# Performance work log

Hardware: AMD Instinct MI355X
Metric: run time of the kernel (lower is better)

## Reference

```python
import jax, jax.numpy as jnp
import numpy as np

# Faithful emulation of SQBnBLinear: SmoothQuant rescale fused with
# bnb Linear8bitLt (threshold=0.0 => no fp16 outlier path):
#   w_sq = weight / scales ; x_sq = x * scales
#   row-wise absmax int8 quantization of both x (per token) and w (per out row)
#   int8 GEMM, then dequant with (ax * aw / 127^2), plus bias / scales.

B, S, D = 4, 2048, 4096

def setup_inputs() -> dict:
    key = jax.random.key(0)
    k1, k2, k3, k4 = jax.random.split(key, 4)
    x = jax.random.normal(k1, (B, S, D), dtype=jnp.float32)
    weight = jax.random.normal(k2, (D, D), dtype=jnp.float32) * 0.02
    bias = jax.random.normal(k3, (D,), dtype=jnp.float32) * 0.02
    # SmoothQuant scales are positive per-input-channel factors
    scales = jax.random.uniform(k4, (D,), dtype=jnp.float32, minval=0.5, maxval=2.0)
    return {"x": x, "weight": weight, "bias": bias, "scales": scales}

def _quantize_rowwise(t):
    # symmetric per-row (last-dim) absmax int8 quantization
    absmax = jnp.max(jnp.abs(t), axis=-1, keepdims=True)
    absmax = jnp.maximum(absmax, 1e-8)
    q = jnp.clip(jnp.round(t * (127.0 / absmax)), -127.0, 127.0)
    return q, absmax

def reference(x, weight, bias, scales):
    # __init__: fold SmoothQuant scales into weight and bias
    w_sq = weight / scales            # [out, in] / [in]
    b_sq = bias / scales              # valid because in_features == out_features
    # forward: rescale input (mul_ by scales)
    x_sq = x * scales                 # [B, S, in]
    # LLM.int8() with threshold=0.0: pure int8 path
    qx, ax = _quantize_rowwise(x_sq)  # qx [B,S,in], ax [B,S,1]
    qw, aw = _quantize_rowwise(w_sq)  # qw [out,in], aw [out,1]
    acc = jnp.einsum('bsi,oi->bso', qx, qw)  # int accumulate (emulated in fp32)
    out = acc * (ax / 127.0) * (aw[:, 0] / 127.0) + b_sq
    return out
```

## Files before the change

kernel.cpp:

```cpp
#include <hip/hip_runtime.h>
#include <stdint.h>

#define DDIM 4096
#define MTOK 8192
#define KTILES (DDIM / 128)

typedef __attribute__((ext_vector_type(4))) int i32x4;
typedef __attribute__((ext_vector_type(16))) int i32x16;

__device__ __forceinline__ void async16(const void* g, void* l) {
    __builtin_amdgcn_global_load_lds(
        (const __attribute__((address_space(1))) unsigned int*)g,
        (__attribute__((address_space(3))) unsigned int*)l,
        16, 0, 0);
}

__global__ __launch_bounds__(256) void quant_all(
    const float* __restrict__ x, const float* __restrict__ weight,
    const float* __restrict__ scales,
    signed char* __restrict__ qx, float* __restrict__ sx,
    signed char* __restrict__ qw, float* __restrict__ sw,
    const float* __restrict__ bias, float* __restrict__ bq)
{
    __shared__ float red[4];
    const int tid = threadIdx.x;
    const bool is_x = blockIdx.x < MTOK;
    const int row = is_x ? blockIdx.x : (blockIdx.x - MTOK);
    const float* src = is_x ? (x + (size_t)row * DDIM) : (weight + (size_t)row * DDIM);
    signed char* q = is_x ? qx : qw;
    float* srow = is_x ? sx : sw;

    const float4* s4 = (const float4*)scales;
    const float4* x4 = (const float4*)src;

    float4 v[4];
    float am = 0.0f;
#pragma unroll
    for (int j = 0; j < 4; ++j) {
        float4 a = x4[tid + j * 256];
        float4 s = s4[tid + j * 256];
        float4 r;
        if (is_x) { r.x = a.x * s.x; r.y = a.y * s.y; r.z = a.z * s.z; r.w = a.w * s.w; }
        else      { r.x = a.x / s.x; r.y = a.y / s.y; r.z = a.z / s.z; r.w = a.w / s.w; }
        v[j] = r;
        am = fmaxf(am, fmaxf(fmaxf(fabsf(r.x), fabsf(r.y)),
                             fmaxf(fabsf(r.z), fabsf(r.w))));
    }
#pragma unroll
    for (int off = 32; off > 0; off >>= 1)
        am = fmaxf(am, __shfl_xor(am, off, 64));
    if ((tid & 63) == 0) red[tid >> 6] = am;
    __syncthreads();
    am = fmaxf(fmaxf(red[0], red[1]), fmaxf(red[2], red[3]));
    am = fmaxf(am, 1e-8f);

    const float sc = 127.0f / am;
    uint32_t* qrow = (uint32_t*)(q + (size_t)row * DDIM);
#pragma unroll
    for (int j = 0; j < 4; ++j) {
        int q0 = (int)fminf(127.0f, fmaxf(-127.0f, rintf(v[j].x * sc)));
        int q1 = (int)fminf(127.0f, fmaxf(-127.0f, rintf(v[j].y * sc)));
        int q2 = (int)fminf(127.0f, fmaxf(-127.0f, rintf(v[j].z * sc)));
        int q3 = (int)fminf(127.0f, fmaxf(-127.0f, rintf(v[j].w * sc)));
        qrow[tid + j * 256] = (uint32_t)(q0 & 0xff) | ((uint32_t)(q1 & 0xff) << 8) |
                              ((uint32_t)(q2 & 0xff) << 16) | ((uint32_t)(q3 & 0xff) << 24);
    }
    if (tid == 0) {
        srow[row] = am * (1.0f / 127.0f);
        if (!is_x) bq[row] = bias[row] / scales[row];
    }
}

__global__ __launch_bounds__(512, 2) void gemm_i8(
    const signed char* __restrict__ qx, const signed char* __restrict__ qw,
    const float* __restrict__ sx, const float* __restrict__ sw,
    const float* __restrict__ bq, float* __restrict__ out)
{
    __shared__ __align__(16) signed char sA[2][256 * 128];
    __shared__ __align__(16) signed char sB[2][256 * 128];

    const int K = DDIM, N = DDIM;
    const int tid  = threadIdx.x;
    const int bm   = blockIdx.y;
    const int bn   = blockIdx.x;
    const int wave = tid >> 6;
    const int lane = tid & 63;
    const int wm   = (wave >> 2) << 7;
    const int wn   = (wave & 3) << 6;
    const int r5   = lane & 31;
    const int hi   = lane >> 5;

    const signed char* Ab = qx + (size_t)bm * 256 * K;
    const signed char* Bb = qw + (size_t)bn * 256 * K;

    const int srow = tid >> 3;
    const int cir  = tid & 7;

    int roff[4];
#pragma unroll
    for (int kq = 0; kq < 4; ++kq)
        roff[kq] = (((kq * 2 + hi) ^ (r5 & 7)) << 4);

    i32x16 acc[4][2] = {};

#pragma unroll
    for (int c = 0; c < 4; ++c) {
        const int row = srow + 64 * c;
        const int kc  = cir ^ (row & 7);
        const int p   = tid * 16 + c * 8192;
        async16(Ab + (size_t)row * K + kc * 16, &sA[0][p]);
        async16(Bb + (size_t)row * K + kc * 16, &sB[0][p]);
    }

    for (int kt = 0; kt < KTILES; ++kt) {
        const int cur = kt & 1;

        if (kt + 1 < KTILES) {
            const int k0n = (kt + 1) * 128;
#pragma unroll
            for (int c = 0; c < 4; ++c) {
                const int row = srow + 64 * c;
                const int kc  = cir ^ (row & 7);
                const int p   = tid * 16 + c * 8192;
                async16(Ab + (size_t)row * K + k0n + kc * 16, &sA[cur ^ 1][p]);
                async16(Bb + (size_t)row * K + k0n + kc * 16, &sB[cur ^ 1][p]);
            }
            asm volatile("s_waitcnt vmcnt(8)" ::: "memory");
        } else {
            asm volatile("s_waitcnt vmcnt(0)" ::: "memory");
        }
        __builtin_amdgcn_s_barrier();
        __builtin_amdgcn_sched_barrier(0);

        const signed char* sAc = sA[cur];
        const signed char* sBc = sB[cur];

#pragma unroll
        for (int p = 0; p < 4; ++p) {
            i32x4 a0 = *(const i32x4*)&sAc[(wm +      r5) * 128 + roff[p]];
            i32x4 a1 = *(const i32x4*)&sAc[(wm + 32 + r5) * 128 + roff[p]];
            i32x4 a2 = *(const i32x4*)&sAc[(wm + 64 + r5) * 128 + roff[p]];
            i32x4 a3 = *(const i32x4*)&sAc[(wm + 96 + r5) * 128 + roff[p]];
            i32x4 b0 = *(const i32x4*)&sBc[(wn +      r5) * 128 + roff[p]];
            i32x4 b1 = *(const i32x4*)&sBc[(wn + 32 + r5) * 128 + roff[p]];

            __builtin_amdgcn_s_barrier();

            __builtin_amdgcn_s_setprio(1);
            acc[0][0] = __builtin_amdgcn_mfma_i32_32x32x32_i8(a0, b0, acc[0][0], 0, 0, 0);
            acc[0][1] = __builtin_amdgcn_mfma_i32_32x32x32_i8(a0, b1, acc[0][1], 0, 0, 0);
            acc[1][0] = __builtin_amdgcn_mfma_i32_32x32x32_i8(a1, b0, acc[1][0], 0, 0, 0);
            acc[1][1] = __builtin_amdgcn_mfma_i32_32x32x32_i8(a1, b1, acc[1][1], 0, 0, 0);
            acc[2][0] = __builtin_amdgcn_mfma_i32_32x32x32_i8(a2, b0, acc[2][0], 0, 0, 0);
            acc[2][1] = __builtin_amdgcn_mfma_i32_32x32x32_i8(a2, b1, acc[2][1], 0, 0, 0);
            acc[3][0] = __builtin_amdgcn_mfma_i32_32x32x32_i8(a3, b0, acc[3][0], 0, 0, 0);
            acc[3][1] = __builtin_amdgcn_mfma_i32_32x32x32_i8(a3, b1, acc[3][1], 0, 0, 0);
            __builtin_amdgcn_s_setprio(0);

            if (p < 3) __builtin_amdgcn_s_barrier();
        }
    }

#pragma unroll
    for (int mi = 0; mi < 4; ++mi) {
        const int mbase = bm * 256 + wm + mi * 32 + 4 * hi;
        float sxv[16];
#pragma unroll
        for (int r = 0; r < 16; ++r)
            sxv[r] = sx[mbase + (r & 3) + 8 * (r >> 2)];
#pragma unroll
        for (int nj = 0; nj < 2; ++nj) {
            const int n = bn * 256 + wn + nj * 32 + r5;
            const float swn = sw[n];
            const float bqn = bq[n];
#pragma unroll
            for (int r = 0; r < 16; ++r) {
                const int m = mbase + (r & 3) + 8 * (r >> 2);
                out[(size_t)m * N + n] = (float)acc[mi][nj][r] * sxv[r] * swn + bqn;
            }
        }
    }
}

extern "C" void kernel_launch(void* const* d_in, const int* in_sizes, int n_in,
                              void* d_out, int out_size, void* d_ws, size_t ws_size,
                              hipStream_t stream) {
    const float* x      = (const float*)d_in[0];
    const float* weight = (const float*)d_in[1];
    const float* bias   = (const float*)d_in[2];
    const float* scales = (const float*)d_in[3];
    float* out = (float*)d_out;

    char* ws = (char*)d_ws;
    signed char* qx = (signed char*)ws;
    signed char* qw = (signed char*)(ws + 33554432);
    float* sx = (float*)(ws + 50331648);
    float* sw = (float*)(ws + 50364416);
    float* bq = (float*)(ws + 50380800);

    quant_all<<<MTOK + DDIM, 256, 0, stream>>>(x, weight, scales, qx, sx, qw, sw, bias, bq);

    dim3 grid(DDIM / 256, MTOK / 256);
    gemm_i8<<<grid, 512, 0, stream>>>(qx, qw, sx, sw, bq, out);
}
```

Before: 422.9 us.

## Switch int8 GEMM to a 4-stage K=64 async ring with one barrier per tile

Replaces the double-buffered K=128 shared-memory pipeline with a four-slot ring of K=64 tiles that prefetches three tiles ahead. The XOR swizzle is adapted to 64-byte rows. Each tile now needs one barrier instead of several. All LDS fragment reads are issued up front, and the first MFMA group starts after a partial lgkmcnt wait, so LDS latency overlaps with matrix math. Total LDS use stays the same, but there are twice as many loop iterations, each with smaller tiles, and the manual vmcnt/lgkmcnt accounting must stay exact.

Measured after the change: 404.2 us. -4.4%, faster.

```diff
diff --git a/kernel.cpp b/kernel.cpp
--- a/kernel.cpp
+++ b/kernel.cpp
@@ -3,7 +3,7 @@
 
 #define DDIM 4096
 #define MTOK 8192
-#define KTILES (DDIM / 128)
+#define NT64 (DDIM / 64)
 
 typedef __attribute__((ext_vector_type(4))) int i32x4;
 typedef __attribute__((ext_vector_type(16))) int i32x16;
@@ -76,8 +76,8 @@
     const float* __restrict__ sx, const float* __restrict__ sw,
     const float* __restrict__ bq, float* __restrict__ out)
 {
-    __shared__ __align__(16) signed char sA[2][256 * 128];
-    __shared__ __align__(16) signed char sB[2][256 * 128];
+    __shared__ __align__(16) signed char sA[4][256 * 64];
+    __shared__ __align__(16) signed char sB[4][256 * 64];
 
     const int K = DDIM, N = DDIM;
     const int tid  = threadIdx.x;
@@ -89,77 +89,95 @@
     const int wn   = (wave & 3) << 6;
     const int r5   = lane & 31;
     const int hi   = lane >> 5;
+    const int xr   = (r5 >> 1) & 3;
 
     const signed char* Ab = qx + (size_t)bm * 256 * K;
     const signed char* Bb = qw + (size_t)bn * 256 * K;
 
-    const int srow = tid >> 3;
-    const int cir  = tid & 7;
-
-    int roff[4];
-#pragma unroll
-    for (int kq = 0; kq < 4; ++kq)
-        roff[kq] = (((kq * 2 + hi) ^ (r5 & 7)) << 4);
+    const int g_row = tid >> 2;
+    const int kc    = (tid & 3) ^ ((tid >> 3) & 3);
+    const int dst0  = tid * 16;
+
+    const int off0 = (((0 * 2 + hi) ^ xr) << 4);
+    const int off1 = (((1 * 2 + hi) ^ xr) << 4);
+    const int rA0 = (wm +      r5) * 64;
+    const int rA1 = (wm + 32 + r5) * 64;
+    const int rA2 = (wm + 64 + r5) * 64;
+    const int rA3 = (wm + 96 + r5) * 64;
+    const int rB0 = (wn +      r5) * 64;
+    const int rB1 = (wn + 32 + r5) * 64;
 
     i32x16 acc[4][2] = {};
 
-#pragma unroll
-    for (int c = 0; c < 4; ++c) {
-        const int row = srow + 64 * c;
-        const int kc  = cir ^ (row & 7);
-        const int p   = tid * 16 + c * 8192;
-        async16(Ab + (size_t)row * K + kc * 16, &sA[0][p]);
-        async16(Bb + (size_t)row * K + kc * 16, &sB[0][p]);
-    }
-
-    for (int kt = 0; kt < KTILES; ++kt) {
-        const int cur = kt & 1;
-
-        if (kt + 1 < KTILES) {
-            const int k0n = (kt + 1) * 128;
-#pragma unroll
-            for (int c = 0; c < 4; ++c) {
-                const int row = srow + 64 * c;
-                const int kc  = cir ^ (row & 7);
-                const int p   = tid * 16 + c * 8192;
-                async16(Ab + (size_t)row * K + k0n + kc * 16, &sA[cur ^ 1][p]);
-                async16(Bb + (size_t)row * K + k0n + kc * 16, &sB[cur ^ 1][p]);
-            }
-            asm volatile("s_waitcnt vmcnt(8)" ::: "memory");
-        } else {
-            asm volatile("s_waitcnt vmcnt(0)" ::: "memory");
-        }
+#define STAGE(t) do {                                                        \
+        const int _s = (t) & 3;                                              \
+        const size_t _k = (size_t)(t) * 64 + kc * 16;                        \
+        async16(Ab + (size_t)g_row         * K + _k, &sA[_s][dst0]);         \
+        async16(Ab + (size_t)(g_row + 128) * K + _k, &sA[_s][dst0 + 8192]);  \
+        async16(Bb + (size_t)g_row         * K + _k, &sB[_s][dst0]);         \
+        async16(Bb + (size_t)(g_row + 128) * K + _k, &sB[_s][dst0 + 8192]);  \
+    } while (0)
+
+    STAGE(0);
+    STAGE(1);
+    STAGE(2);
+
+    for (int h = 0; h < NT64; ++h) {
+        if (h <= NT64 - 3)      asm volatile("s_waitcnt vmcnt(8)" ::: "memory");
+        else if (h == NT64 - 2) asm volatile("s_waitcnt vmcnt(4)" ::: "memory");
+        else                    asm volatile("s_waitcnt vmcnt(0)" ::: "memory");
         __builtin_amdgcn_s_barrier();
         __builtin_amdgcn_sched_barrier(0);
 
-        const signed char* sAc = sA[cur];
-        const signed char* sBc = sB[cur];
-
-#pragma unroll
-        for (int p = 0; p < 4; ++p) {
-            i32x4 a0 = *(const i32x4*)&sAc[(wm +      r5) * 128 + roff[p]];
-            i32x4 a1 = *(const i32x4*)&sAc[(wm + 32 + r5) * 128 + roff[p]];
-            i32x4 a2 = *(const i32x4*)&sAc[(wm + 64 + r5) * 128 + roff[p]];
-            i32x4 a3 = *(const i32x4*)&sAc[(wm + 96 + r5) * 128 + roff[p]];
-            i32x4 b0 = *(const i32x4*)&sBc[(wn +      r5) * 128 + roff[p]];
-            i32x4 b1 = *(const i32x4*)&sBc[(wn + 32 + r5) * 128 + roff[p]];
-
-            __builtin_amdgcn_s_barrier();
-
-            __builtin_amdgcn_s_setprio(1);
-            acc[0][0] = __builtin_amdgcn_mfma_i32_32x32x32_i8(a0, b0, acc[0][0], 0, 0, 0);
-            acc[0][1] = __builtin_amdgcn_mfma_i32_32x32x32_i8(a0, b1, acc[0][1], 0, 0, 0);
-            acc[1][0] = __builtin_amdgcn_mfma_i32_32x32x32_i8(a1, b0, acc[1][0], 0, 0, 0);
-            acc[1][1] = __builtin_amdgcn_mfma_i32_32x32x32_i8(a1, b1, acc[1][1], 0, 0, 0);
-            acc[2][0] = __builtin_amdgcn_mfma_i32_32x32x32_i8(a2, b0, acc[2][0], 0, 0, 0);
-            acc[2][1] = __builtin_amdgcn_mfma_i32_32x32x32_i8(a2, b1, acc[2][1], 0, 0, 0);
-            acc[3][0] = __builtin_amdgcn_mfma_i32_32x32x32_i8(a3, b0, acc[3][0], 0, 0, 0);
-            acc[3][1] = __builtin_amdgcn_mfma_i32_32x32x32_i8(a3, b1, acc[3][1], 0, 0, 0);
-            __builtin_amdgcn_s_setprio(0);
-
-            if (p < 3) __builtin_amdgcn_s_barrier();
-        }
-    }
+        const signed char* a = sA[h & 3];
+        const signed char* b = sB[h & 3];
+
+        i32x4 a00 = *(const i32x4*)&a[rA0 + off0];
+        i32x4 a10 = *(const i32x4*)&a[rA1 + off0];
+        i32x4 a20 = *(const i32x4*)&a[rA2 + off0];
+        i32x4 a30 = *(const i32x4*)&a[rA3 + off0];
+        i32x4 b00 = *(const i32x4*)&b[rB0 + off0];
+        i32x4 b10 = *(const i32x4*)&b[rB1 + off0];
+        __builtin_amdgcn_sched_barrier(0);
+        i32x4 a01 = *(const i32x4*)&a[rA0 + off1];
+        i32x4 a11 = *(const i32x4*)&a[rA1 + off1];
+        i32x4 a21 = *(const i32x4*)&a[rA2 + off1];
+        i32x4 a31 = *(const i32x4*)&a[rA3 + off1];
+        i32x4 b01 = *(const i32x4*)&b[rB0 + off1];
+        i32x4 b11 = *(const i32x4*)&b[rB1 + off1];
+        __builtin_amdgcn_sched_barrier(0);
+
+        if (h + 3 < NT64) STAGE(h + 3);
+        __builtin_amdgcn_sched_barrier(0);
+
+        asm volatile("s_waitcnt lgkmcnt(6)" ::: "memory");
+        __builtin_amdgcn_sched_barrier(0);
+        __builtin_amdgcn_s_setprio(1);
+        acc[0][0] = __builtin_amdgcn_mfma_i32_32x32x32_i8(a00, b00, acc[0][0], 0, 0, 0);
+        acc[0][1] = __builtin_amdgcn_mfma_i32_32x32x32_i8(a00, b10, acc[0][1], 0, 0, 0);
+        acc[1][0] = __builtin_amdgcn_mfma_i32_32x32x32_i8(a10, b00, acc[1][0], 0, 0, 0);
+        acc[1][1] = __builtin_amdgcn_mfma_i32_32x32x32_i8(a10, b10, acc[1][1], 0, 0, 0);
+        acc[2][0] = __builtin_amdgcn_mfma_i32_32x32x32_i8(a20, b00, acc[2][0], 0, 0, 0);
+        acc[2][1] = __builtin_amdgcn_mfma_i32_32x32x32_i8(a20, b10, acc[2][1], 0, 0, 0);
+        acc[3][0] = __builtin_amdgcn_mfma_i32_32x32x32_i8(a30, b00, acc[3][0], 0, 0, 0);
+        acc[3][1] = __builtin_amdgcn_mfma_i32_32x32x32_i8(a30, b10, acc[3][1], 0, 0, 0);
+        __builtin_amdgcn_s_setprio(0);
+        __builtin_amdgcn_sched_barrier(0);
+
+        asm volatile("s_waitcnt lgkmcnt(0)" ::: "memory");
+        __builtin_amdgcn_sched_barrier(0);
+        __builtin_amdgcn_s_setprio(1);
+        acc[0][0] = __builtin_amdgcn_mfma_i32_32x32x32_i8(a01, b01, acc[0][0], 0, 0, 0);
+        acc[0][1] = __builtin_amdgcn_mfma_i32_32x32x32_i8(a01, b11, acc[0][1], 0, 0, 0);
+        acc[1][0] = __builtin_amdgcn_mfma_i32_32x32x32_i8(a11, b01, acc[1][0], 0, 0, 0);
+        acc[1][1] = __builtin_amdgcn_mfma_i32_32x32x32_i8(a11, b11, acc[1][1], 0, 0, 0);
+        acc[2][0] = __builtin_amdgcn_mfma_i32_32x32x32_i8(a21, b01, acc[2][0], 0, 0, 0);
+        acc[2][1] = __builtin_amdgcn_mfma_i32_32x32x32_i8(a21, b11, acc[2][1], 0, 0, 0);
+        acc[3][0] = __builtin_amdgcn_mfma_i32_32x32x32_i8(a31, b01, acc[3][0], 0, 0, 0);
+        acc[3][1] = __builtin_amdgcn_mfma_i32_32x32x32_i8(a31, b11, acc[3][1], 0, 0, 0);
+        __builtin_amdgcn_s_setprio(0);
+    }
+#undef STAGE
 
 #pragma unroll
     for (int mi = 0; mi < 4; ++mi) {
```
